# Optimization experiments

Measured on AMD Instinct MI355X. Metric: run time of the kernel, lower is better.

Reference implementation:

```python
import jax, jax.numpy as jnp
import numpy as np

N, E, S, G = 20000, 60000, 3000, 128
EAD = 5
DIMS = [(16, 32), (32, 64), (64, 64)]  # NNConv (M_in, M_out) per layer
HID = 128  # edge-MLP hidden
FC_IN = 64 + 8  # conv output + raw continuous feats


def setup_inputs() -> dict:
    key = jax.random.key(0)
    ks = iter(jax.random.split(key, 64))
    inp = {}
    inp['x'] = jax.random.normal(next(ks), (N, 24), jnp.float32)
    inp['edge_index'] = jax.random.randint(next(ks), (2, E), 0, N)
    inp['edge_attr'] = jax.random.uniform(next(ks), (E, EAD), jnp.float32)
    inp['node_to_subgraph'] = jnp.sort(jax.random.randint(next(ks), (N,), 0, S))
    inp['subgraph_to_graph'] = jnp.sort(jax.random.randint(next(ks), (S,), 0, G))
    for i, (mi, mo) in enumerate(DIMS):
        inp[f'conv{i}_w1'] = jax.random.normal(next(ks), (EAD, HID), jnp.float32) / np.sqrt(EAD)
        inp[f'conv{i}_b1'] = jnp.zeros((HID,), jnp.float32)
        inp[f'conv{i}_w2'] = jax.random.normal(next(ks), (HID, mi * mo), jnp.float32) / np.sqrt(HID * mi)
        inp[f'conv{i}_b2'] = jnp.zeros((mi * mo,), jnp.float32)
        inp[f'conv{i}_root'] = jax.random.normal(next(ks), (mi, mo), jnp.float32) / np.sqrt(mi)
        inp[f'conv{i}_bias'] = jnp.zeros((mo,), jnp.float32)
    dims_fc = [(FC_IN, FC_IN // 2), (FC_IN // 2, FC_IN // 4), (FC_IN // 4, 1)]
    for i, (di, do) in enumerate(dims_fc):
        inp[f'fc{i+1}_w'] = jax.random.normal(next(ks), (di, do), jnp.float32) / np.sqrt(di)
        inp[f'fc{i+1}_b'] = jnp.zeros((do,), jnp.float32)
    return inp


def _nnconv(x, src, dst, ea, w1, b1, w2, b2, root, bias):
    # edge MLP -> per-edge weight matrix [E, M_in, M_out]
    h = jax.nn.relu(ea @ w1 + b1)
    mi, mo = root.shape
    W = (h @ w2 + b2).reshape(-1, mi, mo)
    msg = jnp.einsum('ei,eio->eo', x[src], W)  # gather + per-edge matmul
    agg = jax.ops.segment_sum(msg, dst, num_segments=x.shape[0])  # scatter-add
    return agg + x @ root + bias


def _mean_pool(x, seg, num):
    s = jax.ops.segment_sum(x, seg, num_segments=num)
    c = jax.ops.segment_sum(jnp.ones((x.shape[0], 1), x.dtype), seg, num_segments=num)
    return s / jnp.maximum(c, 1.0)


def _forward(x, edge_index, edge_attr, node_to_subgraph, subgraph_to_graph, convs, fcs):
    src, dst = edge_index[0], edge_index[1]
    xi = x[:, :16]
    for p in convs:
        xi = jax.nn.elu(_nnconv(xi, src, dst, edge_attr, *p))
    x_cont = x[:, 16:]
    xc = jnp.concatenate([xi, x_cont], axis=1)  # [N, 72]
    xs = _mean_pool(xc, node_to_subgraph, S)    # [S, 72]
    xg = _mean_pool(xs, subgraph_to_graph, G)   # [G, 72]
    (w1, b1), (w2, b2), (w3, b3) = fcs
    xg = jax.nn.elu(xg @ w1 + b1)
    xg = jax.nn.elu(xg @ w2 + b2)
    return (xg @ w3 + b3).reshape(-1)


def reference(x, edge_index, edge_attr, node_to_subgraph, subgraph_to_graph,
              conv0_w1, conv0_b1, conv0_w2, conv0_b2, conv0_root, conv0_bias,
              conv1_w1, conv1_b1, conv1_w2, conv1_b2, conv1_root, conv1_bias,
              conv2_w1, conv2_b1, conv2_w2, conv2_b2, conv2_root, conv2_bias,
              fc1_w, fc1_b, fc2_w, fc2_b, fc3_w, fc3_b):
    convs = [
        (conv0_w1, conv0_b1, conv0_w2, conv0_b2, conv0_root, conv0_bias),
        (conv1_w1, conv1_b1, conv1_w2, conv1_b2, conv1_root, conv1_bias),
        (conv2_w1, conv2_b1, conv2_w2, conv2_b2, conv2_root, conv2_bias),
    ]
    fcs = [(fc1_w, fc1_b), (fc2_w, fc2_b), (fc3_w, fc3_b)]
    return _forward(x, edge_index, edge_attr, node_to_subgraph, subgraph_to_graph, convs, fcs)
```

## Files before the change

### kernel.cpp

```cpp
#include <hip/hip_runtime.h>
#include <hip/hip_bf16.h>
#include <cmath>

#define NN 20000
#define NE 60000
#define NS 3000
#define NG 128
#define HIDN 128
#define SCB 79
#define TILES 938
#define SLST 3840000

typedef float f32x16 __attribute__((ext_vector_type(16)));
typedef _Float16 f16x8 __attribute__((ext_vector_type(8)));

__device__ __forceinline__ float eluf(float v) { return v > 0.f ? v : expm1f(v); }

__device__ __forceinline__ void gload_lds16(const void* g, void* l) {
    __builtin_amdgcn_global_load_lds(
        (const __attribute__((address_space(1))) unsigned int*)g,
        (__attribute__((address_space(3))) unsigned int*)l, 16, 0, 0);
}

__device__ __forceinline__ void vmwait0() {
    asm volatile("s_waitcnt vmcnt(0)" ::: "memory");
}
__device__ __forceinline__ void vmwait8() {
    asm volatile("s_waitcnt vmcnt(8)" ::: "memory");
}

__global__ void k_hist(const int* __restrict__ dst, int* __restrict__ deg) {
    int e = blockIdx.x * 256 + threadIdx.x;
    if (e < NE) atomicAdd(&deg[dst[e]], 1);
}

__global__ void k_scan1(const int* __restrict__ deg, int* __restrict__ bsum) {
    __shared__ int s[256];
    const int t = threadIdx.x;
    int i = blockIdx.x * 256 + t;
    s[t] = (i < NN) ? deg[i] : 0;
    __syncthreads();
#pragma unroll
    for (int off = 128; off > 0; off >>= 1) {
        if (t < off) s[t] += s[t + off];
        __syncthreads();
    }
    if (t == 0) bsum[blockIdx.x] = s[0];
}

__global__ void k_scan2(const int* __restrict__ bsum, int* __restrict__ boff) {
    __shared__ int s[SCB];
    const int t = threadIdx.x;
    if (t < SCB) s[t] = bsum[t];
    __syncthreads();
    if (t == 0) {
        int acc = 0;
        for (int i = 0; i < SCB; ++i) { int v = s[i]; s[i] = acc; acc += v; }
    }
    __syncthreads();
    if (t < SCB) boff[t] = s[t];
}

__global__ void k_scan3(const int* __restrict__ deg, const int* __restrict__ boff,
                        int* __restrict__ rowptr) {
    __shared__ int s[256];
    const int t = threadIdx.x;
    int i = blockIdx.x * 256 + t;
    int v = (i < NN) ? deg[i] : 0;
    s[t] = v;
    __syncthreads();
#pragma unroll
    for (int off = 1; off < 256; off <<= 1) {
        int a = (t >= off) ? s[t - off] : 0;
        __syncthreads();
        s[t] += a;
        __syncthreads();
    }
    if (i < NN) rowptr[i + 1] = boff[blockIdx.x] + s[t];
    if (i == 0) rowptr[0] = 0;
}

__global__ void k_scatter(const int* __restrict__ src, const int* __restrict__ dst,
                          const int* __restrict__ rowptr, int* __restrict__ tmp,
                          int* __restrict__ eord, int* __restrict__ srcS) {
    int e = blockIdx.x * 256 + threadIdx.x;
    if (e >= NE) return;
    int d = dst[e];
    int pos = rowptr[d] + atomicAdd(&tmp[d], 1);
    eord[pos] = e;
    srcS[pos] = src[e];
}

#define PRE_N0 66048
#define PRE_N1 264192
#define PRE_N2 528384
#define PRE_N3 320000
#define PRE_TOT (PRE_N0 + PRE_N1 + PRE_N2 + PRE_N3)

__global__ void k_prep(const float* __restrict__ w20, const float* __restrict__ b20,
                       const float* __restrict__ w21, const float* __restrict__ b21,
                       const float* __restrict__ w22, const float* __restrict__ b22,
                       const float* __restrict__ x,
                       _Float16* __restrict__ w2t0, _Float16* __restrict__ w2t1,
                       _Float16* __restrict__ w2t2, _Float16* __restrict__ x16h) {
    int idx = blockIdx.x * 256 + threadIdx.x;
    if (idx < PRE_N0) {
        constexpr int KP = 129 * 16, KF = 128 * 16, MO = 32;
        int o = idx / KP, kg = idx % KP;
        float v = (kg < KF) ? w20[(size_t)kg * MO + o] : b20[(kg - KF) * MO + o];
        w2t0[idx] = (_Float16)v;
    } else if (idx < PRE_N0 + PRE_N1) {
        int i2 = idx - PRE_N0;
        constexpr int KP = 129 * 32, KF = 128 * 32, MO = 64;
        int o = i2 / KP, kg = i2 % KP;
        float v = (kg < KF) ? w21[(size_t)kg * MO + o] : b21[(kg - KF) * MO + o];
        w2t1[i2] = (_Float16)v;
    } else if (idx < PRE_N0 + PRE_N1 + PRE_N2) {
        int i2 = idx - PRE_N0 - PRE_N1;
        constexpr int KP = 129 * 64, KF = 128 * 64, MO = 64;
        int o = i2 / KP, kg = i2 % KP;
        float v = (kg < KF) ? w22[(size_t)kg * MO + o] : b22[(kg - KF) * MO + o];
        w2t2[i2] = (_Float16)v;
    } else if (idx < PRE_TOT) {
        int i2 = idx - PRE_N0 - PRE_N1 - PRE_N2;
        int n = i2 >> 4, i = i2 & 15;
        x16h[i2] = (_Float16)x[n * 24 + i];
    }
}

template <int MI, int MO, int XS>
__global__ __launch_bounds__(256, 2) void k_edgeB(
    const _Float16* __restrict__ xi, const float* __restrict__ ea,
    const float* __restrict__ w1, const float* __restrict__ b1,
    const _Float16* __restrict__ w2t, const int* __restrict__ srcS,
    const int* __restrict__ eord, _Float16* __restrict__ msg) {
    constexpr int PH  = MI / 16;
    constexpr int KP  = 129 * MI;
    constexpr int NT  = MO / 32;
    constexpr int CH  = 16 / (PH * NT);
    constexpr int NCH = 64 / CH;
    static_assert(CH * PH * NT == 16, "ITEMS must be 16");
    static_assert(NCH % 2 == 0, "chunk loop unrolled x2");

    __shared__ __align__(16) _Float16 sb[2][2][16 * 512];

    const int lane = threadIdx.x & 63;
    const int w    = threadIdx.x >> 6;
    const int mg   = w & 1;
    const int kh   = w >> 1;
    const int lo5  = lane & 31;
    const int hi   = lane >> 5;
    const int e0   = blockIdx.x * 128 + mg * 64;
    const int kb   = kh * 64;

    const int rc0 = min(e0 + lo5, NE - 1);
    const int rc1 = min(e0 + 32 + lo5, NE - 1);
    const int s0 = srcS[rc0];
    const int s1 = srcS[rc1];

    float ea0[5], ea1[5];
    {
        const int eo0 = eord[rc0], eo1 = eord[rc1];
#pragma unroll
        for (int d = 0; d < 5; ++d) {
            ea0[d] = ea[eo0 * 5 + d];
            ea1[d] = ea[eo1 * 5 + d];
        }
    }

    f16x8 xr0[PH], xr1[PH];
    {
        const _Float16* xb0 = xi + (size_t)s0 * XS + hi * 8;
        const _Float16* xb1 = xi + (size_t)s1 * XS + hi * 8;
#pragma unroll
        for (int p = 0; p < PH; ++p) {
            xr0[p] = *reinterpret_cast<const f16x8*>(xb0 + p * 16);
            xr1[p] = *reinterpret_cast<const f16x8*>(xb1 + p * 16);
        }
    }

    f32x16 acc[2][NT];
#pragma unroll
    for (int m = 0; m < 2; ++m)
#pragma unroll
        for (int n = 0; n < NT; ++n)
#pragma unroll
            for (int i = 0; i < 16; ++i) acc[m][n][i] = 0.f;

    auto stage = [&](int buf, int kc) {
#pragma unroll
        for (int jj = 0; jj < 8; ++jj) {
            const int j  = mg + jj * 2;
            const int n  = j % NT;
            const int kp = j / NT;
            const int p  = kp % PH;
            const int kk = kp / PH;
            gload_lds16(w2t + (size_t)(n * 32 + lo5) * KP
                            + (size_t)(kb + kc + kk) * MI + p * 16 + hi * 8,
                        &sb[kh][buf][j * 512]);
        }
    };

    auto calc_h = [&](int kc, _Float16* h0, _Float16* h1) {
#pragma unroll
        for (int kk = 0; kk < CH; ++kk) {
            const int k = kb + kc + kk;
            const float c0 = w1[0 * HIDN + k], c1 = w1[1 * HIDN + k],
                        c2 = w1[2 * HIDN + k], c3 = w1[3 * HIDN + k],
                        c4 = w1[4 * HIDN + k], bb = b1[k];
            float t0 = bb, t1 = bb;
            t0 = fmaf(ea0[0], c0, t0); t1 = fmaf(ea1[0], c0, t1);
            t0 = fmaf(ea0[1], c1, t0); t1 = fmaf(ea1[1], c1, t1);
            t0 = fmaf(ea0[2], c2, t0); t1 = fmaf(ea1[2], c2, t1);
            t0 = fmaf(ea0[3], c3, t0); t1 = fmaf(ea1[3], c3, t1);
            t0 = fmaf(ea0[4], c4, t0); t1 = fmaf(ea1[4], c4, t1);
            h0[kk] = (_Float16)fmaxf(t0, 0.f);
            h1[kk] = (_Float16)fmaxf(t1, 0.f);
        }
    };

    auto compute = [&](int buf, const _Float16* h0, const _Float16* h1) {
        const _Float16* sbc = &sb[kh][buf][0];
#pragma unroll
        for (int kk = 0; kk < CH; ++kk) {
            const _Float16 hv0 = h0[kk];
            const _Float16 hv1 = h1[kk];
            const f16x8 h80 = {hv0, hv0, hv0, hv0, hv0, hv0, hv0, hv0};
            const f16x8 h81 = {hv1, hv1, hv1, hv1, hv1, hv1, hv1, hv1};
#pragma unroll
            for (int p = 0; p < PH; ++p) {
                const f16x8 af0 = xr0[p] * h80;
                const f16x8 af1 = xr1[p] * h81;
#pragma unroll
                for (int n = 0; n < NT; ++n) {
                    const f16x8 bv = *reinterpret_cast<const f16x8*>(
                        &sbc[((kk * PH + p) * NT + n) * 512 + lane * 8]);
                    acc[0][n] = __builtin_amdgcn_mfma_f32_32x32x16_f16(af0, bv, acc[0][n], 0, 0, 0);
                    acc[1][n] = __builtin_amdgcn_mfma_f32_32x32x16_f16(af1, bv, acc[1][n], 0, 0, 0);
                }
            }
        }
    };

    _Float16 hA0[CH], hA1[CH], hB0[CH], hB1[CH];

    stage(0, 0);
    calc_h(0, hA0, hA1);

    for (int c = 0; c < NCH; c += 2) {
        stage(1, (c + 1) * CH);
        calc_h((c + 1) * CH, hB0, hB1);
        vmwait8();
        __builtin_amdgcn_sched_barrier(0);
        __builtin_amdgcn_s_barrier();
        __builtin_amdgcn_sched_barrier(0);
        compute(0, hA0, hA1);
        __builtin_amdgcn_sched_barrier(0);
        __builtin_amdgcn_s_barrier();

        const bool pf = (c + 2 < NCH);
        if (pf) {
            stage(0, (c + 2) * CH);
            calc_h((c + 2) * CH, hA0, hA1);
            vmwait8();
        } else {
            vmwait0();
        }
        __builtin_amdgcn_sched_barrier(0);
        __builtin_amdgcn_s_barrier();
        __builtin_amdgcn_sched_barrier(0);
        compute(1, hB0, hB1);
        __builtin_amdgcn_sched_barrier(0);
        __builtin_amdgcn_s_barrier();
    }

    if (kh == 1) {
#pragma unroll
        for (int p = 0; p < PH; ++p) {
#pragma unroll
            for (int n = 0; n < NT; ++n) {
                const f16x8 bv = *reinterpret_cast<const f16x8*>(
                    w2t + (size_t)(n * 32 + lo5) * KP + (size_t)128 * MI + p * 16 + hi * 8);
                acc[0][n] = __builtin_amdgcn_mfma_f32_32x32x16_f16(xr0[p], bv, acc[0][n], 0, 0, 0);
                acc[1][n] = __builtin_amdgcn_mfma_f32_32x32x16_f16(xr1[p], bv, acc[1][n], 0, 0, 0);
            }
        }
    }

    __syncthreads();
    float* red = reinterpret_cast<float*>(&sb[0][0][0]);
    if (kh == 1) {
#pragma unroll
        for (int m = 0; m < 2; ++m)
#pragma unroll
            for (int n = 0; n < NT; ++n) {
                float* d = red + (size_t)((mg * 2 + m) * NT + n) * 1024 + lane;
#pragma unroll
                for (int i = 0; i < 16; ++i) d[i * 64] = acc[m][n][i];
            }
    }
    __syncthreads();
    if (kh == 0) {
#pragma unroll
        for (int m = 0; m < 2; ++m)
#pragma unroll
            for (int n = 0; n < NT; ++n) {
                const float* s = red + (size_t)((mg * 2 + m) * NT + n) * 1024 + lane;
#pragma unroll
                for (int i = 0; i < 16; ++i) acc[m][n][i] += s[i * 64];
            }
#pragma unroll
        for (int m = 0; m < 2; ++m)
#pragma unroll
            for (int q = 0; q < 4; ++q)
#pragma unroll
                for (int a2 = 0; a2 < 4; ++a2) {
                    const int e = e0 + m * 32 + 4 * hi + 8 * q + a2;
                    if (e < NE) {
#pragma unroll
                        for (int n = 0; n < NT; ++n)
                            msg[(size_t)e * MO + n * 32 + lo5] =
                                (_Float16)acc[m][n][4 * q + a2];
                    }
                }
    }
}

template <int MI, int MO, int XS>
__global__ __launch_bounds__(768, 3) void k_edgeP(
    const _Float16* __restrict__ xi, const float* __restrict__ ea,
    const float* __restrict__ w1, const float* __restrict__ b1,
    const _Float16* __restrict__ w2t, const int* __restrict__ srcS,
    const int* __restrict__ eord, _Float16* __restrict__ msgP, int tilesPerBlock) {
    constexpr int PH = MI / 16;
    constexpr int KP = 129 * MI;
    constexpr int NT = MO / 32;
    constexpr int MAXITEMS = 17 * PH * NT;

    __shared__ __align__(16) _Float16 sb[MAXITEMS * 512];

    const int t    = threadIdx.x;
    const int lane = t & 63;
    const int w    = t >> 6;
    const int lo5  = lane & 31;
    const int hi   = lane >> 5;

    const int sl    = blockIdx.y;
    const int k0    = sl * 16;
    const int kspan = (sl == 7) ? 17 : 16;
    const int items = kspan * PH * NT;

    for (int j = w; j < items; j += 12) {
        const int kk  = j / (PH * NT);
        const int rem = j % (PH * NT);
        const int p   = rem / NT;
        const int n   = rem % NT;
        gload_lds16(w2t + (size_t)(n * 32 + lo5) * KP
                        + (size_t)(k0 + kk) * MI + p * 16 + hi * 8,
                    &sb[j * 512]);
    }
    vmwait0();
    __syncthreads();

    _Float16* msgS = msgP + (size_t)sl * SLST;
    const int tile0 = blockIdx.x * tilesPerBlock;
    const int tile1 = min(tile0 + tilesPerBlock, TILES);

    for (int tile = tile0 + w; tile < tile1; tile += 12) {
        const int e0  = tile * 64;
        const int rc0 = min(e0 + lo5, NE - 1);
        const int rc1 = min(e0 + 32 + lo5, NE - 1);
        const int s0 = srcS[rc0];
        const int s1 = srcS[rc1];

        float ea0[5], ea1[5];
        {
            const int eo0 = eord[rc0], eo1 = eord[rc1];
#pragma unroll
            for (int d = 0; d < 5; ++d) {
                ea0[d] = ea[eo0 * 5 + d];
                ea1[d] = ea[eo1 * 5 + d];
            }
        }

        f16x8 xr0[PH], xr1[PH];
        {
            const _Float16* xb0 = xi + (size_t)s0 * XS + hi * 8;
            const _Float16* xb1 = xi + (size_t)s1 * XS + hi * 8;
#pragma unroll
            for (int p = 0; p < PH; ++p) {
                xr0[p] = *reinterpret_cast<const f16x8*>(xb0 + p * 16);
                xr1[p] = *reinterpret_cast<const f16x8*>(xb1 + p * 16);
            }
        }

        f32x16 acc[2][NT];
#pragma unroll
        for (int m = 0; m < 2; ++m)
#pragma unroll
            for (int n = 0; n < NT; ++n)
#pragma unroll
                for (int i = 0; i < 16; ++i) acc[m][n][i] = 0.f;

        for (int kk2 = 0; kk2 < kspan; ++kk2) {
            const int k = k0 + kk2;
            _Float16 hv0, hv1;
            if (k < 128) {
                const float c0 = w1[0 * HIDN + k], c1 = w1[1 * HIDN + k],
                            c2 = w1[2 * HIDN + k], c3 = w1[3 * HIDN + k],
                            c4 = w1[4 * HIDN + k], bb = b1[k];
                float t0 = bb, t1 = bb;
                t0 = fmaf(ea0[0], c0, t0); t1 = fmaf(ea1[0], c0, t1);
                t0 = fmaf(ea0[1], c1, t0); t1 = fmaf(ea1[1], c1, t1);
                t0 = fmaf(ea0[2], c2, t0); t1 = fmaf(ea1[2], c2, t1);
                t0 = fmaf(ea0[3], c3, t0); t1 = fmaf(ea1[3], c3, t1);
                t0 = fmaf(ea0[4], c4, t0); t1 = fmaf(ea1[4], c4, t1);
                hv0 = (_Float16)fmaxf(t0, 0.f);
                hv1 = (_Float16)fmaxf(t1, 0.f);
            } else {
                hv0 = (_Float16)1.0f;
                hv1 = (_Float16)1.0f;
            }
            const f16x8 h80 = {hv0, hv0, hv0, hv0, hv0, hv0, hv0, hv0};
            const f16x8 h81 = {hv1, hv1, hv1, hv1, hv1, hv1, hv1, hv1};
#pragma unroll
            for (int p = 0; p < PH; ++p) {
                const f16x8 af0 = xr0[p] * h80;
                const f16x8 af1 = xr1[p] * h81;
#pragma unroll
                for (int n = 0; n < NT; ++n) {
                    const f16x8 bv = *reinterpret_cast<const f16x8*>(
                        &sb[((kk2 * PH + p) * NT + n) * 512 + lane * 8]);
                    acc[0][n] = __builtin_amdgcn_mfma_f32_32x32x16_f16(af0, bv, acc[0][n], 0, 0, 0);
                    acc[1][n] = __builtin_amdgcn_mfma_f32_32x32x16_f16(af1, bv, acc[1][n], 0, 0, 0);
                }
            }
        }

#pragma unroll
        for (int m = 0; m < 2; ++m)
#pragma unroll
            for (int q = 0; q < 4; ++q)
#pragma unroll
                for (int a2 = 0; a2 < 4; ++a2) {
                    const int e = e0 + m * 32 + 4 * hi + 8 * q + a2;
                    if (e < NE) {
#pragma unroll
                        for (int n = 0; n < NT; ++n)
                            msgS[(size_t)e * MO + n * 32 + lo5] =
                                (_Float16)acc[m][n][4 * q + a2];
                    }
                }
    }
}

template <int MI, int MO, int XS>
__global__ void k_agg(const _Float16* __restrict__ msg, const int* __restrict__ rowptr,
                      const float* __restrict__ xi, const float* __restrict__ root,
                      const float* __restrict__ bias, float* __restrict__ out,
                      _Float16* __restrict__ outh) {
    int idx = blockIdx.x * 256 + threadIdx.x;
    if (idx >= NN * MO) return;
    int n = idx / MO, o = idx % MO;
    float s = bias[o];
#pragma unroll
    for (int i = 0; i < MI; ++i) s = fmaf(xi[(size_t)n * XS + i], root[i * MO + o], s);
    const int j0 = rowptr[n], j1 = rowptr[n + 1];
    for (int j = j0; j < j1; ++j) s += (float)msg[(size_t)j * MO + o];
    float r = eluf(s);
    out[idx] = r;
    outh[idx] = (_Float16)r;
}

__global__ void k_agg_pool(const _Float16* __restrict__ msgP, int nsl,
                           const int* __restrict__ rowptr,
                           const float* __restrict__ xi, const float* __restrict__ root,
                           const float* __restrict__ bias, const float* __restrict__ x,
                           const int* __restrict__ n2s, float* __restrict__ xs_sum,
                           float* __restrict__ cs) {
    int idx = blockIdx.x * 256 + threadIdx.x;
    if (idx >= NN * 72) return;
    int n = idx / 72, o = idx % 72;
    float r;
    if (o < 64) {
        float s = bias[o];
#pragma unroll
        for (int i = 0; i < 64; ++i) s = fmaf(xi[(size_t)n * 64 + i], root[i * 64 + o], s);
        const int j0 = rowptr[n], j1 = rowptr[n + 1];
        for (int j = j0; j < j1; ++j) {
            const _Float16* mp = msgP + (size_t)j * 64 + o;
            for (int sl = 0; sl < nsl; ++sl) s += (float)mp[(size_t)sl * SLST];
        }
        r = eluf(s);
    } else {
        r = x[n * 24 + 16 + (o - 64)];
    }
    const int sg = n2s[n];
    atomicAdd(&xs_sum[sg * 72 + o], r);
    if (o == 0) atomicAdd(&cs[sg], 1.f);
}

__global__ void k_pool_g(const float* __restrict__ xs_sum, const float* __restrict__ cs,
                         const int* __restrict__ s2g, float* __restrict__ xg_sum,
                         float* __restrict__ cg) {
    int idx = blockIdx.x * 256 + threadIdx.x;
    if (idx >= NS * 72) return;
    int s = idx / 72, j = idx % 72;
    float v = xs_sum[s * 72 + j] / fmaxf(cs[s], 1.f);
    int g = s2g[s];
    atomicAdd(&xg_sum[g * 72 + j], v);
    if (j == 0) atomicAdd(&cg[g], 1.f);
}

__global__ void k_fc(const float* __restrict__ xg_sum, const float* __restrict__ cg,
                     const float* __restrict__ w1, const float* __restrict__ b1,
                     const float* __restrict__ w2, const float* __restrict__ b2,
                     const float* __restrict__ w3, const float* __restrict__ b3,
                     float* __restrict__ out) {
    int g = threadIdx.x;
    if (g >= NG) return;
    float inv = 1.f / fmaxf(cg[g], 1.f);
    float v[72];
#pragma unroll
    for (int j = 0; j < 72; ++j) v[j] = xg_sum[g * 72 + j] * inv;
    float h1[36];
#pragma unroll
    for (int o = 0; o < 36; ++o) {
        float s = b1[o];
#pragma unroll
        for (int i = 0; i < 72; ++i) s = fmaf(v[i], w1[i * 36 + o], s);
        h1[o] = eluf(s);
    }
    float h2[18];
#pragma unroll
    for (int o = 0; o < 18; ++o) {
        float s = b2[o];
#pragma unroll
        for (int i = 0; i < 36; ++i) s = fmaf(h1[i], w2[i * 18 + o], s);
        h2[o] = eluf(s);
    }
    float s = b3[0];
#pragma unroll
    for (int i = 0; i < 18; ++i) s = fmaf(h2[i], w3[i], s);
    out[g] = s;
}

extern "C" void kernel_launch(void* const* d_in, const int* in_sizes, int n_in,
                              void* d_out, int out_size, void* d_ws, size_t ws_size,
                              hipStream_t stream) {
    const float* x   = (const float*)d_in[0];
    const int*   ei  = (const int*)d_in[1];
    const float* ea  = (const float*)d_in[2];
    const int*   n2s = (const int*)d_in[3];
    const int*   s2g = (const int*)d_in[4];
    const int* src = ei;
    const int* dst = ei + NE;

    const float* cw1[3]   = {(const float*)d_in[5],  (const float*)d_in[11], (const float*)d_in[17]};
    const float* cb1[3]   = {(const float*)d_in[6],  (const float*)d_in[12], (const float*)d_in[18]};
    const float* cw2[3]   = {(const float*)d_in[7],  (const float*)d_in[13], (const float*)d_in[19]};
    const float* cb2[3]   = {(const float*)d_in[8],  (const float*)d_in[14], (const float*)d_in[20]};
    const float* croot[3] = {(const float*)d_in[9],  (const float*)d_in[15], (const float*)d_in[21]};
    const float* cbias[3] = {(const float*)d_in[10], (const float*)d_in[16], (const float*)d_in[22]};
    const float* fc1w = (const float*)d_in[23];
    const float* fc1b = (const float*)d_in[24];
    const float* fc2w = (const float*)d_in[25];
    const float* fc2b = (const float*)d_in[26];
    const float* fc3w = (const float*)d_in[27];
    const float* fc3b = (const float*)d_in[28];

    char* W = (char*)d_ws;
    float*    xiA   = (float*)(W);
    float*    xiB   = (float*)(W + 5120000);
    _Float16* xiAh  = (_Float16*)(W + 10240000);
    _Float16* xiBh  = (_Float16*)(W + 12800000);
    _Float16* x16h  = (_Float16*)(W + 15360000);
    float*    xs_sum= (float*)(W + 16000000);
    float*    cs    = (float*)(W + 16864000);
    float*    xg_sum= (float*)(W + 16876000);
    float*    cg    = (float*)(W + 16912864);
    int*      deg   = (int*)(W + 16913376);
    int*      tmp   = (int*)(W + 16993376);
    _Float16* w2t0  = (_Float16*)(W + 17073376);
    _Float16* w2t1  = (_Float16*)(W + 17205472);
    _Float16* w2t2  = (_Float16*)(W + 17733856);
    int*      rowptr= (int*)(W + 18790624);
    int*      eord  = (int*)(W + 18870640);
    int*      srcS  = (int*)(W + 19110640);
    int*      bsum  = (int*)(W + 19350640);
    int*      boff  = (int*)(W + 19350960);
    _Float16* msgP  = (_Float16*)(W + 19351296);
    const size_t NEED_P = 19351296ull + 8ull * 7680000ull;
    const bool useP = (ws_size >= NEED_P);
    _Float16* msg = msgP;

    hipMemsetAsync(xs_sum, 0, 1073376, stream);

    k_hist<<<(NE + 255) / 256, 256, 0, stream>>>(dst, deg);
    k_scan1<<<SCB, 256, 0, stream>>>(deg, bsum);
    k_scan2<<<1, 128, 0, stream>>>(bsum, boff);
    k_scan3<<<SCB, 256, 0, stream>>>(deg, boff, rowptr);
    k_scatter<<<(NE + 255) / 256, 256, 0, stream>>>(src, dst, rowptr, tmp, eord, srcS);

    k_prep<<<(PRE_TOT + 255) / 256, 256, 0, stream>>>(
        cw2[0], cb2[0], cw2[1], cb2[1], cw2[2], cb2[2], x, w2t0, w2t1, w2t2, x16h);

    const int EB = (NE + 127) / 128;

    k_edgeB<16, 32, 16><<<EB, 256, 0, stream>>>(x16h, ea, cw1[0], cb1[0], w2t0, srcS, eord, msg);
    k_agg<16, 32, 24><<<(NN * 32 + 255) / 256, 256, 0, stream>>>(msg, rowptr, x, croot[0], cbias[0], xiB, xiBh);

    k_edgeB<32, 64, 32><<<EB, 256, 0, stream>>>(xiBh, ea, cw1[1], cb1[1], w2t1, srcS, eord, msg);
    k_agg<32, 64, 32><<<(NN * 64 + 255) / 256, 256, 0, stream>>>(msg, rowptr, xiB, croot[1], cbias[1], xiA, xiAh);

    if (useP) {
        const int XB = 32;
        const int TPB = (TILES + XB - 1) / XB;
        k_edgeP<64, 64, 64><<<dim3(XB, 8), 768, 0, stream>>>(
            xiAh, ea, cw1[2], cb1[2], w2t2, srcS, eord, msgP, TPB);
        k_agg_pool<<<(NN * 72 + 255) / 256, 256, 0, stream>>>(
            msgP, 8, rowptr, xiA, croot[2], cbias[2], x, n2s, xs_sum, cs);
    } else {
        k_edgeB<64, 64, 64><<<EB, 256, 0, stream>>>(xiAh, ea, cw1[2], cb1[2], w2t2, srcS, eord, msg);
        k_agg_pool<<<(NN * 72 + 255) / 256, 256, 0, stream>>>(
            msg, 1, rowptr, xiA, croot[2], cbias[2], x, n2s, xs_sum, cs);
    }

    k_pool_g<<<(NS * 72 + 255) / 256, 256, 0, stream>>>(xs_sum, cs, s2g, xg_sum, cg);
    k_fc<<<1, 128, 0, stream>>>(xg_sum, cg, fc1w, fc1b, fc2w, fc2b, fc3w, fc3b, (float*)d_out);
}
```

Measured before the change: 302.0 us.

## Generalize K-sliced edge kernel to all conv layers with separate slice reduction

Templatizes the K-split edge kernel on slice size, slice count and wave count, and uses it for layers 0 and 1 as well as layer 2 instead of the block-tiled edge kernel. Partial messages from the K slices are now summed by a dedicated vectorized reduction kernel into slice 0, so the aggregation kernels read one message buffer rather than looping over slices per neighbor. This spreads the edge-MLP weight GEMM across more blocks with weights resident in LDS. In exchange it adds extra kernel launches and a full pass writing and reading partial-message buffers.

```diff
diff --git a/kernel.cpp b/kernel.cpp
--- a/kernel.cpp
+++ b/kernel.cpp
@@ -140,7 +140,6 @@
     constexpr int CH  = 16 / (PH * NT);
     constexpr int NCH = 64 / CH;
     static_assert(CH * PH * NT == 16, "ITEMS must be 16");
-    static_assert(NCH % 2 == 0, "chunk loop unrolled x2");
 
     __shared__ __align__(16) _Float16 sb[2][2][16 * 512];
 
@@ -326,8 +325,8 @@
     }
 }
 
-template <int MI, int MO, int XS>
-__global__ __launch_bounds__(768, 3) void k_edgeP(
+template <int MI, int MO, int XS, int KSL, int NSL, int WV>
+__global__ __launch_bounds__(WV * 64, WV / 4) void k_edgeP(
     const _Float16* __restrict__ xi, const float* __restrict__ ea,
     const float* __restrict__ w1, const float* __restrict__ b1,
     const _Float16* __restrict__ w2t, const int* __restrict__ srcS,
@@ -335,7 +334,8 @@
     constexpr int PH = MI / 16;
     constexpr int KP = 129 * MI;
     constexpr int NT = MO / 32;
-    constexpr int MAXITEMS = 17 * PH * NT;
+    constexpr int LASTK = 129 - (NSL - 1) * KSL;
+    constexpr int MAXITEMS = LASTK * PH * NT;
 
     __shared__ __align__(16) _Float16 sb[MAXITEMS * 512];
 
@@ -346,11 +346,11 @@
     const int hi   = lane >> 5;
 
     const int sl    = blockIdx.y;
-    const int k0    = sl * 16;
-    const int kspan = (sl == 7) ? 17 : 16;
+    const int k0    = sl * KSL;
+    const int kspan = (sl == NSL - 1) ? LASTK : KSL;
     const int items = kspan * PH * NT;
 
-    for (int j = w; j < items; j += 12) {
+    for (int j = w; j < items; j += WV) {
         const int kk  = j / (PH * NT);
         const int rem = j % (PH * NT);
         const int p   = rem / NT;
@@ -362,11 +362,11 @@
     vmwait0();
     __syncthreads();
 
-    _Float16* msgS = msgP + (size_t)sl * SLST;
+    _Float16* msgS = msgP + (size_t)sl * ((size_t)NE * MO);
     const int tile0 = blockIdx.x * tilesPerBlock;
     const int tile1 = min(tile0 + tilesPerBlock, TILES);
 
-    for (int tile = tile0 + w; tile < tile1; tile += 12) {
+    for (int tile = tile0 + w; tile < tile1; tile += WV) {
         const int e0  = tile * 64;
         const int rc0 = min(e0 + lo5, NE - 1);
         const int rc1 = min(e0 + 32 + lo5, NE - 1);
@@ -454,6 +454,23 @@
     }
 }
 
+template <int NSL>
+__global__ void k_red(_Float16* __restrict__ msgP) {
+    int idx = blockIdx.x * 256 + threadIdx.x;
+    if (idx >= NE * 8) return;
+    float a[8] = {0, 0, 0, 0, 0, 0, 0, 0};
+#pragma unroll
+    for (int sl = 0; sl < NSL; ++sl) {
+        const f16x8 v = *reinterpret_cast<const f16x8*>(msgP + (size_t)sl * SLST + (size_t)idx * 8);
+#pragma unroll
+        for (int i = 0; i < 8; ++i) a[i] += (float)v[i];
+    }
+    f16x8 r;
+#pragma unroll
+    for (int i = 0; i < 8; ++i) r[i] = (_Float16)a[i];
+    *reinterpret_cast<f16x8*>(msgP + (size_t)idx * 8) = r;
+}
+
 template <int MI, int MO, int XS>
 __global__ void k_agg(const _Float16* __restrict__ msg, const int* __restrict__ rowptr,
                       const float* __restrict__ xi, const float* __restrict__ root,
@@ -472,8 +489,7 @@
     outh[idx] = (_Float16)r;
 }
 
-__global__ void k_agg_pool(const _Float16* __restrict__ msgP, int nsl,
-                           const int* __restrict__ rowptr,
+__global__ void k_agg_pool(const _Float16* __restrict__ msg, const int* __restrict__ rowptr,
                            const float* __restrict__ xi, const float* __restrict__ root,
                            const float* __restrict__ bias, const float* __restrict__ x,
                            const int* __restrict__ n2s, float* __restrict__ xs_sum,
@@ -487,10 +503,7 @@
 #pragma unroll
         for (int i = 0; i < 64; ++i) s = fmaf(xi[(size_t)n * 64 + i], root[i * 64 + o], s);
         const int j0 = rowptr[n], j1 = rowptr[n + 1];
-        for (int j = j0; j < j1; ++j) {
-            const _Float16* mp = msgP + (size_t)j * 64 + o;
-            for (int sl = 0; sl < nsl; ++sl) s += (float)mp[(size_t)sl * SLST];
-        }
+        for (int j = j0; j < j1; ++j) s += (float)msg[(size_t)j * 64 + o];
         r = eluf(s);
     } else {
         r = x[n * 24 + 16 + (o - 64)];
@@ -606,24 +619,40 @@
         cw2[0], cb2[0], cw2[1], cb2[1], cw2[2], cb2[2], x, w2t0, w2t1, w2t2, x16h);
 
     const int EB = (NE + 127) / 128;
-
-    k_edgeB<16, 32, 16><<<EB, 256, 0, stream>>>(x16h, ea, cw1[0], cb1[0], w2t0, srcS, eord, msg);
-    k_agg<16, 32, 24><<<(NN * 32 + 255) / 256, 256, 0, stream>>>(msg, rowptr, x, croot[0], cbias[0], xiB, xiBh);
-
-    k_edgeB<32, 64, 32><<<EB, 256, 0, stream>>>(xiBh, ea, cw1[1], cb1[1], w2t1, srcS, eord, msg);
-    k_agg<32, 64, 32><<<(NN * 64 + 255) / 256, 256, 0, stream>>>(msg, rowptr, xiB, croot[1], cbias[1], xiA, xiAh);
+    const int REDB = (NE * 8 + 255) / 256;
 
     if (useP) {
-        const int XB = 32;
-        const int TPB = (TILES + XB - 1) / XB;
-        k_edgeP<64, 64, 64><<<dim3(XB, 8), 768, 0, stream>>>(
-            xiAh, ea, cw1[2], cb1[2], w2t2, srcS, eord, msgP, TPB);
+        {
+            const int XB = 118, TPB = 8;
+            k_edgeP<16, 32, 16, 129, 1, 8><<<dim3(XB, 1), 512, 0, stream>>>(
+                x16h, ea, cw1[0], cb1[0], w2t0, srcS, eord, msg, TPB);
+        }
+        k_agg<16, 32, 24><<<(NN * 32 + 255) / 256, 256, 0, stream>>>(msg, rowptr, x, croot[0], cbias[0], xiB, xiBh);
+
+        {
+            const int XB = 64, TPB = (TILES + 63) / 64;
+            k_edgeP<32, 64, 32, 32, 4, 12><<<dim3(XB, 4), 768, 0, stream>>>(
+                xiBh, ea, cw1[1], cb1[1], w2t1, srcS, eord, msgP, TPB);
+        }
+        k_red<4><<<REDB, 256, 0, stream>>>(msgP);
+        k_agg<32, 64, 32><<<(NN * 64 + 255) / 256, 256, 0, stream>>>(msg, rowptr, xiB, croot[1], cbias[1], xiA, xiAh);
+
+        {
+            const int XB = 32, TPB = (TILES + 31) / 32;
+            k_edgeP<64, 64, 64, 16, 8, 12><<<dim3(XB, 8), 768, 0, stream>>>(
+                xiAh, ea, cw1[2], cb1[2], w2t2, srcS, eord, msgP, TPB);
+        }
+        k_red<8><<<REDB, 256, 0, stream>>>(msgP);
         k_agg_pool<<<(NN * 72 + 255) / 256, 256, 0, stream>>>(
-            msgP, 8, rowptr, xiA, croot[2], cbias[2], x, n2s, xs_sum, cs);
+            msg, rowptr, xiA, croot[2], cbias[2], x, n2s, xs_sum, cs);
     } else {
+        k_edgeB<16, 32, 16><<<EB, 256, 0, stream>>>(x16h, ea, cw1[0], cb1[0], w2t0, srcS, eord, msg);
+        k_agg<16, 32, 24><<<(NN * 32 + 255) / 256, 256, 0, stream>>>(msg, rowptr, x, croot[0], cbias[0], xiB, xiBh);
+        k_edgeB<32, 64, 32><<<EB, 256, 0, stream>>>(xiBh, ea, cw1[1], cb1[1], w2t1, srcS, eord, msg);
+        k_agg<32, 64, 32><<<(NN * 64 + 255) / 256, 256, 0, stream>>>(msg, rowptr, xiB, croot[1], cbias[1], xiA, xiAh);
         k_edgeB<64, 64, 64><<<EB, 256, 0, stream>>>(xiAh, ea, cw1[2], cb1[2], w2t2, srcS, eord, msg);
         k_agg_pool<<<(NN * 72 + 255) / 256, 256, 0, stream>>>(
-            msg, 1, rowptr, xiA, croot[2], cbias[2], x, n2s, xs_sum, cs);
+            msg, rowptr, xiA, croot[2], cbias[2], x, n2s, xs_sum, cs);
     }
 
     k_pool_g<<<(NS * 72 + 255) / 256, 256, 0, stream>>>(xs_sum, cs, s2g, xg_sum, cg);
```

New measurement: 275.7 us, median of 2. 1.1x faster.
